# Performance work log

Measured on AMD Instinct MI355X. Metric: run time of the kernel, lower is better.

The kernel has to match this reference:

```python
import jax, jax.numpy as jnp
import numpy as np

C = 512
GROUPS = 32
EPS = 1e-6


def setup_inputs() -> dict:
    key = jax.random.key(0)
    ks = jax.random.split(key, 10)
    B, H, W = 4, 64, 64
    s = 1.0 / np.sqrt(C)
    return {
        "x": jax.random.normal(ks[0], (B, C, H, W), dtype=jnp.float32),
        "gn_weight": jnp.ones((C,), jnp.float32),
        "gn_bias": jnp.zeros((C,), jnp.float32),
        "Wq": jax.random.normal(ks[1], (C, C), jnp.float32) * s,
        "bq": jnp.zeros((C,), jnp.float32),
        "Wk": jax.random.normal(ks[2], (C, C), jnp.float32) * s,
        "bk": jnp.zeros((C,), jnp.float32),
        "Wv": jax.random.normal(ks[3], (C, C), jnp.float32) * s,
        "bv": jnp.zeros((C,), jnp.float32),
        "Wo": jax.random.normal(ks[4], (C, C), jnp.float32) * s,
        "bo": jnp.zeros((C,), jnp.float32),
    }


def _group_norm(x, weight, bias):
    B, Ch, H, W = x.shape
    xg = x.reshape(B, GROUPS, Ch // GROUPS, H, W)
    mean = jnp.mean(xg, axis=(2, 3, 4), keepdims=True)
    var = jnp.var(xg, axis=(2, 3, 4), keepdims=True)
    xg = (xg - mean) * jax.lax.rsqrt(var + EPS)
    h = xg.reshape(B, Ch, H, W)
    return h * weight[None, :, None, None] + bias[None, :, None, None]


def reference(x, gn_weight, gn_bias, Wq, bq, Wk, bk, Wv, bv, Wo, bo):
    B, Ch, H, W = x.shape
    h = _group_norm(x, gn_weight, gn_bias)
    # [B, N, C] with N = H*W spatial tokens
    h = h.reshape(B, Ch, H * W).transpose(0, 2, 1)
    q = h @ Wq.T + bq
    k = h @ Wk.T + bk
    v = h @ Wv.T + bv
    scale = 1.0 / jnp.sqrt(jnp.asarray(Ch, x.dtype))
    scores = jnp.einsum("bnc,bmc->bnm", q, k) * scale  # [B, N, N]
    attn = jax.nn.softmax(scores, axis=-1)
    out = jnp.einsum("bnm,bmc->bnc", attn, v)
    out = out @ Wo.T + bo  # Dropout(0.0) is identity
    out = out.transpose(0, 2, 1).reshape(B, Ch, H, W)
    return x + out
```

## Files before the change

### kernel.cpp

```cpp
#include <hip/hip_runtime.h>
#include <hip/hip_bf16.h>

typedef __attribute__((ext_vector_type(8))) short bf16x8;
typedef __attribute__((ext_vector_type(4))) short bf16x4;
typedef __attribute__((ext_vector_type(4))) float f32x4;

__device__ __forceinline__ short f2bf(float f){
  __hip_bfloat16 h = __float2bfloat16(f);
  return __builtin_bit_cast(short, h);
}
__device__ __forceinline__ float bf2f(short s){
  unsigned u = ((unsigned)(unsigned short)s) << 16;
  return __builtin_bit_cast(float, u);
}

__device__ __forceinline__ void gload_lds16(const short* g, char* l){
  __builtin_amdgcn_global_load_lds(
      (const __attribute__((address_space(1))) void*)g,
      (__attribute__((address_space(3))) void*)l, 16, 0, 0);
}

__global__ __launch_bounds__(256) void gn_stats(const float* __restrict__ x,
                                                float* __restrict__ stats){
  int b = blockIdx.x >> 5, g = blockIdx.x & 31;
  const float4* p = (const float4*)(x + ((long long)b*512 + g*16)*4096);
  float s = 0.f, s2 = 0.f;
  for (int i = threadIdx.x; i < 16384; i += 256){
    float4 v = p[i];
    s  += v.x + v.y + v.z + v.w;
    s2 += v.x*v.x + v.y*v.y + v.z*v.z + v.w*v.w;
  }
  #pragma unroll
  for (int o = 32; o; o >>= 1){ s += __shfl_xor(s, o); s2 += __shfl_xor(s2, o); }
  __shared__ float rs[4], rs2[4];
  int wid = threadIdx.x >> 6;
  if ((threadIdx.x & 63) == 0){ rs[wid] = s; rs2[wid] = s2; }
  __syncthreads();
  if (threadIdx.x == 0){
    float S  = rs[0]+rs[1]+rs[2]+rs[3];
    float S2 = rs2[0]+rs2[1]+rs2[2]+rs2[3];
    float mean = S * (1.f/65536.f);
    float var  = S2 * (1.f/65536.f) - mean*mean;
    stats[blockIdx.x*2]   = mean;
    stats[blockIdx.x*2+1] = rsqrtf(var + 1e-6f);
  }
}

__global__ __launch_bounds__(256) void gn_apply(const float* __restrict__ x,
                                                const float* __restrict__ stats,
                                                const float* __restrict__ gw,
                                                const float* __restrict__ gb,
                                                short* __restrict__ h){
  __shared__ float tile[128][65];
  int b  = blockIdx.y;
  int n0 = blockIdx.x * 64;
  int t  = threadIdx.x;
  const float* xb = x + (long long)b*512*4096;
  for (int cc = 0; cc < 4; cc++){
    int c0 = cc*128;
    #pragma unroll
    for (int r = 0; r < 128; r += 4){
      int c = r + (t >> 6);
      tile[c][t & 63] = xb[(long long)(c0+c)*4096 + n0 + (t & 63)];
    }
    __syncthreads();
    int n = t >> 2, cp = (t & 3)*32;
    short tmp[32];
    #pragma unroll
    for (int j = 0; j < 32; j++){
      int c = c0 + cp + j;
      float mean = stats[(b*32 + (c >> 4))*2];
      float rstd = stats[(b*32 + (c >> 4))*2 + 1];
      float v = (tile[cp+j][n] - mean)*rstd*gw[c] + gb[c];
      tmp[j] = f2bf(v);
    }
    long long ho = ((long long)b*4096 + n0 + n)*512 + c0 + cp;
    #pragma unroll
    for (int j2 = 0; j2 < 4; j2++){
      bf16x8 v8;
      #pragma unroll
      for (int e = 0; e < 8; e++) v8[e] = tmp[j2*8 + e];
      *(bf16x8*)&h[ho + j2*8] = v8;
    }
    __syncthreads();
  }
}

__global__ __launch_bounds__(256) void f2bf_all(
    const float* __restrict__ w0, const float* __restrict__ w1,
    const float* __restrict__ w2, const float* __restrict__ w3,
    short* __restrict__ o0, short* __restrict__ o1,
    short* __restrict__ o2, short* __restrict__ o3){
  int idx = blockIdx.x*256 + threadIdx.x;
  int m = idx >> 15, r = idx & 32767;
  const float* src = (m==0) ? w0 : (m==1) ? w1 : (m==2) ? w2 : w3;
  short* dst       = (m==0) ? o0 : (m==1) ? o1 : (m==2) ? o2 : o3;
  const float4* p = (const float4*)src + (long long)r*2;
  float4 a = p[0], c = p[1];
  bf16x8 v;
  v[0]=f2bf(a.x); v[1]=f2bf(a.y); v[2]=f2bf(a.z); v[3]=f2bf(a.w);
  v[4]=f2bf(c.x); v[5]=f2bf(c.y); v[6]=f2bf(c.z); v[7]=f2bf(c.w);
  *(bf16x8*)&dst[(long long)r*8] = v;
}

__global__ __launch_bounds__(256) void softmax_rows(short* __restrict__ S){
  long long row = blockIdx.x;
  short* p = S + row*4096;
  int t = threadIdx.x;
  bf16x8 v0 = *(bf16x8*)&p[t*16];
  bf16x8 v1 = *(bf16x8*)&p[t*16 + 8];
  float f[16];
  #pragma unroll
  for (int e = 0; e < 8; e++){ f[e] = bf2f(v0[e]); f[8+e] = bf2f(v1[e]); }
  float m = f[0];
  #pragma unroll
  for (int e = 1; e < 16; e++) m = fmaxf(m, f[e]);
  #pragma unroll
  for (int o = 32; o; o >>= 1) m = fmaxf(m, __shfl_xor(m, o));
  __shared__ float red[4];
  int wid = t >> 6;
  if ((t & 63) == 0) red[wid] = m;
  __syncthreads();
  m = fmaxf(fmaxf(red[0], red[1]), fmaxf(red[2], red[3]));
  float s = 0.f;
  #pragma unroll
  for (int e = 0; e < 16; e++){ f[e] = exp2f((f[e]-m)*1.4426950408889634f); s += f[e]; }
  #pragma unroll
  for (int o = 32; o; o >>= 1) s += __shfl_xor(s, o);
  __syncthreads();
  if ((t & 63) == 0) red[wid] = s;
  __syncthreads();
  s = red[0]+red[1]+red[2]+red[3];
  float inv = 1.f/s;
  #pragma unroll
  for (int e = 0; e < 8; e++){ v0[e] = f2bf(f[e]*inv); v1[e] = f2bf(f[8+e]*inv); }
  *(bf16x8*)&p[t*16]     = v0;
  *(bf16x8*)&p[t*16 + 8] = v1;
}

template<int MODE, int BN>
__global__ __launch_bounds__(512, 2) void gemm256(
    const short* __restrict__ A, const short* __restrict__ Bw,
    const float* __restrict__ bias,
    void* __restrict__ outp, const float* __restrict__ resid,
    int M, int Nn, int Kd,
    long long sA, long long sB, long long sO, float scale)
{
  constexpr int BROUNDS = BN/64;
  constexpr int LOADS   = 4 + BROUNDS;
  constexpr int WM = (BN==256) ? 128 : 64;
  constexpr int WN = 64;
  constexpr int WAVES_N = BN/WN;
  constexpr int MF = WM/16, NF = WN/16;
  constexpr int ASZ = 32768, BSZ = BN*128;
  extern __shared__ char smem[];

  const int bz = blockIdx.z;
  const short* Ab = A + bz*sA;
  const short* Bb = Bw + bz*sB;
  const int m0 = blockIdx.x*256, n0 = blockIdx.y*BN;
  const int t = threadIdx.x;
  const int lane = t & 63, wid = t >> 6;
  const int g = lane >> 4, lr = lane & 15;
  const int wr = wid / WAVES_N, wc = wid % WAVES_N;

  const int rsub = t >> 3;
  const int chunkEl = (((t & 7) ^ (rsub & 7))) * 8;
  const short* gA[4]; const short* gB[BROUNDS];
  #pragma unroll
  for (int j = 0; j < 4; j++)
    gA[j] = Ab + (long long)(m0 + j*64 + rsub)*Kd + chunkEl;
  #pragma unroll
  for (int j = 0; j < BROUNDS; j++)
    gB[j] = Bb + (long long)(n0 + j*64 + rsub)*Kd + chunkEl;
  const int tb = t*16;

  const int rowAbyte = (wr*WM + lr)*128;
  const int rowBbyte = (wc*WN + lr)*128;
  const int ch0 = ((g)     ^ (lr & 7)) << 4;
  const int ch1 = ((4 + g) ^ (lr & 7)) << 4;

  f32x4 acc[MF][NF];
  #pragma unroll
  for (int i = 0; i < MF; i++)
    #pragma unroll
    for (int j = 0; j < NF; j++)
      acc[i][j] = f32x4{0.f,0.f,0.f,0.f};

  const int NT = Kd >> 6;

  auto STAGE = [&](int tile, int buf){
    char* base = smem + buf*(ASZ+BSZ);
    const int kt = tile*64;
    #pragma unroll
    for (int j = 0; j < 4; j++)
      gload_lds16(gA[j] + kt, base + j*8192 + tb);
    #pragma unroll
    for (int j = 0; j < BROUNDS; j++)
      gload_lds16(gB[j] + kt, base + ASZ + j*8192 + tb);
  };

  STAGE(0, 0);
  STAGE(1, 1);
  if constexpr (LOADS == 8) asm volatile("s_waitcnt vmcnt(8)" ::: "memory");
  else                      asm volatile("s_waitcnt vmcnt(6)" ::: "memory");
  __builtin_amdgcn_s_barrier();

  for (int it = 0; it < NT; ++it){
    char* base = smem + (it & 1)*(ASZ+BSZ);
    bf16x8 av[MF][2], bv[NF][2];
    #pragma unroll
    for (int ni = 0; ni < NF; ni++){
      bv[ni][0] = *(const bf16x8*)(base + ASZ + rowBbyte + ni*2048 + ch0);
      bv[ni][1] = *(const bf16x8*)(base + ASZ + rowBbyte + ni*2048 + ch1);
    }
    #pragma unroll
    for (int mi = 0; mi < MF; mi++){
      av[mi][0] = *(const bf16x8*)(base + rowAbyte + mi*2048 + ch0);
      av[mi][1] = *(const bf16x8*)(base + rowAbyte + mi*2048 + ch1);
    }
    asm volatile("s_waitcnt lgkmcnt(0)" ::: "memory");
    __builtin_amdgcn_sched_barrier(0);
    __builtin_amdgcn_s_barrier();

    if (it + 2 < NT) STAGE(it + 2, it & 1);

    #pragma unroll
    for (int mi = 0; mi < MF; mi++)
      #pragma unroll
      for (int ni = 0; ni < NF; ni++)
        #pragma unroll
        for (int ks = 0; ks < 2; ks++){
          if constexpr (MODE == 0)
            acc[mi][ni] = __builtin_amdgcn_mfma_f32_16x16x32_bf16(bv[ni][ks], av[mi][ks], acc[mi][ni], 0, 0, 0);
          else
            acc[mi][ni] = __builtin_amdgcn_mfma_f32_16x16x32_bf16(av[mi][ks], bv[ni][ks], acc[mi][ni], 0, 0, 0);
        }

    if (it + 2 < NT){
      if constexpr (LOADS == 8) asm volatile("s_waitcnt vmcnt(8)" ::: "memory");
      else                      asm volatile("s_waitcnt vmcnt(6)" ::: "memory");
    } else {
      asm volatile("s_waitcnt vmcnt(0)" ::: "memory");
    }
    __builtin_amdgcn_s_barrier();
  }

  if constexpr (MODE == 0){
    short* outb = (short*)outp + bz*sO;
    const bool hb = (bias != nullptr);
    #pragma unroll
    for (int mi = 0; mi < MF; mi++){
      int row = m0 + wr*WM + mi*16 + lr;
      #pragma unroll
      for (int ni = 0; ni < NF; ni++){
        int col = n0 + wc*WN + ni*16 + g*4;
        float b0=0.f,b1=0.f,b2=0.f,b3=0.f;
        if (hb){ float4 bb = *(const float4*)&bias[col]; b0=bb.x; b1=bb.y; b2=bb.z; b3=bb.w; }
        bf16x4 pk;
        pk[0] = f2bf((acc[mi][ni][0] + b0)*scale);
        pk[1] = f2bf((acc[mi][ni][1] + b1)*scale);
        pk[2] = f2bf((acc[mi][ni][2] + b2)*scale);
        pk[3] = f2bf((acc[mi][ni][3] + b3)*scale);
        *(bf16x4*)&outb[(long long)row*Nn + col] = pk;
      }
    }
  } else if constexpr (MODE == 1){
    short* outb = (short*)outp + bz*sO;
    #pragma unroll
    for (int ni = 0; ni < NF; ni++){
      int col = n0 + wc*WN + ni*16 + lr;
      float bv2 = bias ? bias[col] : 0.f;
      #pragma unroll
      for (int mi = 0; mi < MF; mi++){
        int row = m0 + wr*WM + mi*16 + g*4;
        bf16x4 pk;
        #pragma unroll
        for (int i = 0; i < 4; i++) pk[i] = f2bf((acc[mi][ni][i] + bv2)*scale);
        *(bf16x4*)&outb[(long long)col*M + row] = pk;
      }
    }
  } else {
    float* outb = (float*)outp + bz*sO;
    const float* rx = resid + bz*sO;
    #pragma unroll
    for (int ni = 0; ni < NF; ni++){
      int col = n0 + wc*WN + ni*16 + lr;
      float bv2 = bias[col];
      #pragma unroll
      for (int mi = 0; mi < MF; mi++){
        int row = m0 + wr*WM + mi*16 + g*4;
        long long off = (long long)col*M + row;
        float4 xr = *(const float4*)&rx[off];
        float4 o;
        o.x = acc[mi][ni][0] + bv2 + xr.x;
        o.y = acc[mi][ni][1] + bv2 + xr.y;
        o.z = acc[mi][ni][2] + bv2 + xr.z;
        o.w = acc[mi][ni][3] + bv2 + xr.w;
        *(float4*)&outb[off] = o;
      }
    }
  }
}

extern "C" void kernel_launch(void* const* d_in, const int* in_sizes, int n_in,
                              void* d_out, int out_size, void* d_ws, size_t ws_size,
                              hipStream_t stream)
{
  const float* x   = (const float*)d_in[0];
  const float* gnw = (const float*)d_in[1];
  const float* gnb = (const float*)d_in[2];
  const float* Wq  = (const float*)d_in[3];
  const float* bq  = (const float*)d_in[4];
  const float* Wk  = (const float*)d_in[5];
  const float* bk  = (const float*)d_in[6];
  const float* Wv  = (const float*)d_in[7];
  const float* bvp = (const float*)d_in[8];
  const float* Wo  = (const float*)d_in[9];
  const float* bo  = (const float*)d_in[10];
  float* out = (float*)d_out;

  char* ws = (char*)d_ws;
  const size_t MB = 1ull << 20;
  short* h    = (short*)(ws);
  short* q    = (short*)(ws + 16*MB);
  short* kmat = (short*)(ws + 32*MB);
  short* vt   = (short*)(ws + 48*MB);
  short* ao   = (short*)(ws + 64*MB);
  short* wqb  = (short*)(ws + 80*MB);
  short* wkb  = wqb + 262144;
  short* wvb  = wkb + 262144;
  short* wob  = wvb + 262144;
  float* stats= (float*)(ws + 82*MB);
  short* S    = (short*)(ws + 84*MB);

  const int LDS256 = 131072, LDS128 = 98304;
  hipFuncSetAttribute(reinterpret_cast<const void*>(&gemm256<0,256>),
                      hipFuncAttributeMaxDynamicSharedMemorySize, LDS256);
  hipFuncSetAttribute(reinterpret_cast<const void*>(&gemm256<0,128>),
                      hipFuncAttributeMaxDynamicSharedMemorySize, LDS128);
  hipFuncSetAttribute(reinterpret_cast<const void*>(&gemm256<1,128>),
                      hipFuncAttributeMaxDynamicSharedMemorySize, LDS128);
  hipFuncSetAttribute(reinterpret_cast<const void*>(&gemm256<2,128>),
                      hipFuncAttributeMaxDynamicSharedMemorySize, LDS128);

  dim3 blk(256);
  dim3 blk512(512);
  gn_stats<<<dim3(128), blk, 0, stream>>>(x, stats);
  gn_apply<<<dim3(64,4), blk, 0, stream>>>(x, stats, gnw, gnb, h);
  f2bf_all<<<dim3(512), blk, 0, stream>>>(Wq, Wk, Wv, Wo, wqb, wkb, wvb, wob);

  const long long sTok = 4096ll*512;
  const float qscale = 0.044194173824159216f;

  gemm256<0,128><<<dim3(16,4,4), blk512, LDS128, stream>>>(h, wqb, bq,  q,    nullptr, 4096, 512, 512, sTok, 0, sTok, qscale);
  gemm256<0,128><<<dim3(16,4,4), blk512, LDS128, stream>>>(h, wkb, bk,  kmat, nullptr, 4096, 512, 512, sTok, 0, sTok, 1.f);
  gemm256<1,128><<<dim3(16,4,4), blk512, LDS128, stream>>>(h, wvb, bvp, vt,   nullptr, 4096, 512, 512, sTok, 0, sTok, 1.f);

  if (ws_size >= 212*MB){
    gemm256<0,256><<<dim3(16,16,4), blk512, LDS256, stream>>>(q, kmat, nullptr, S, nullptr, 4096, 4096, 512, sTok, sTok, 4096ll*4096, 1.f);
    softmax_rows<<<dim3(16384), blk, 0, stream>>>(S);
    gemm256<0,128><<<dim3(16,4,4), blk512, LDS128, stream>>>(S, vt, nullptr, ao, nullptr, 4096, 512, 4096, 4096ll*4096, sTok, sTok, 1.f);
  } else {
    for (int b = 0; b < 4; b++){
      gemm256<0,256><<<dim3(16,16,1), blk512, LDS256, stream>>>(q + b*sTok, kmat + b*sTok, nullptr, S, nullptr, 4096, 4096, 512, 0, 0, 0, 1.f);
      softmax_rows<<<dim3(4096), blk, 0, stream>>>(S);
      gemm256<0,128><<<dim3(16,4,1), blk512, LDS128, stream>>>(S, vt + b*sTok, nullptr, ao + b*sTok, nullptr, 4096, 512, 4096, 0, 0, 0, 1.f);
    }
  }

  gemm256<2,128><<<dim3(16,4,4), blk512, LDS128, stream>>>(ao, wob, bo, out, x, 4096, 512, 512, sTok, 0, sTok, 1.f);
}
```

Measured before the change: 352.7 us.

## Add 8-phase pipelined GEMM kernel for attention score and PV matmuls

Adds a new gemm8p kernel that splits each K-tile into four MFMA quadrants, interleaving LDS reads and async global-to-LDS staging with compute phases separated by barriers and s_setprio. It uses double-buffered LDS with fine-grained vmcnt waits so loads overlap with MFMA work. The QK^T and softmax×V GEMMs now use it in place of gemm256. The hand-scheduled barriers and waitcnt logic add complexity and could stall if the phases are mismatched.

```diff
diff --git a/kernel.cpp b/kernel.cpp
--- a/kernel.cpp
+++ b/kernel.cpp
@@ -136,6 +136,190 @@
   for (int e = 0; e < 8; e++){ v0[e] = f2bf(f[e]*inv); v1[e] = f2bf(f[8+e]*inv); }
   *(bf16x8*)&p[t*16]     = v0;
   *(bf16x8*)&p[t*16 + 8] = v1;
+}
+
+#define READ_A8(QM, BASE) do{                                          \
+  _Pragma("unroll")                                                    \
+  for (int _i = 0; _i < MF2; _i++){                                    \
+    _Pragma("unroll")                                                  \
+    for (int _ks = 0; _ks < 2; _ks++)                                  \
+      av[_i][_ks] = *(const bf16x8*)((BASE) + roA[(QM)*MF2+_i] +       \
+                     (((_ks*4+g) ^ swA[(QM)*MF2+_i])<<4));             \
+  } }while(0)
+
+#define READ_B4(QN, BASE) do{                                          \
+  _Pragma("unroll")                                                    \
+  for (int _j = 0; _j < 2; _j++){                                      \
+    _Pragma("unroll")                                                  \
+    for (int _ks = 0; _ks < 2; _ks++)                                  \
+      bv[(QN)*2+_j][_ks] = *(const bf16x8*)((BASE) + roB[(QN)*2+_j] +  \
+                     (((_ks*4+g) ^ swB[(QN)*2+_j])<<4));               \
+  } }while(0)
+
+#define MFMA_Q(QM, QN) do{                                             \
+  _Pragma("unroll")                                                    \
+  for (int _i = 0; _i < MF2; _i++)                                     \
+    _Pragma("unroll")                                                  \
+    for (int _j = 0; _j < 2; _j++)                                     \
+      _Pragma("unroll")                                                \
+      for (int _ks = 0; _ks < 2; _ks++)                                \
+        acc[(QM)*MF2+_i][(QN)*2+_j] =                                  \
+          __builtin_amdgcn_mfma_f32_16x16x32_bf16(bv[(QN)*2+_j][_ks],  \
+            av[_i][_ks], acc[(QM)*MF2+_i][(QN)*2+_j], 0,0,0);          \
+  }while(0)
+
+#define STAGE_A(BUF, H, KT) do{                                        \
+  char* _d = smem + (BUF)*BUFSZ + (H)*16384 + t*16;                    \
+  const short* _s = pA0 + (H)*128*KdLL + (KT)*64;                      \
+  gload_lds16(_s, _d);                                                 \
+  gload_lds16(_s + 64*KdLL, _d + 8192);                                \
+}while(0)
+
+#define STAGE_B(BUF, H, KT) do{                                        \
+  char* _d = smem + (BUF)*BUFSZ + ABUF + (H)*BHALF + t*16;             \
+  const short* _s = pB0 + (H)*RB*KdLL + (KT)*64;                       \
+  gload_lds16(_s, _d);                                                 \
+  if constexpr (LB == 2) gload_lds16(_s + 64*KdLL, _d + 8192);         \
+}while(0)
+
+#define WAITV_STEADY() do{                                             \
+  if constexpr (LB == 2) asm volatile("s_waitcnt vmcnt(4)" ::: "memory"); \
+  else                   asm volatile("s_waitcnt vmcnt(2)" ::: "memory"); \
+}while(0)
+
+#define PH_BEGIN()                                                     \
+  __builtin_amdgcn_sched_barrier(0);                                   \
+  __builtin_amdgcn_s_barrier();                                        \
+  __builtin_amdgcn_sched_barrier(0);                                   \
+  asm volatile("s_waitcnt lgkmcnt(0)" ::: "memory");                   \
+  __builtin_amdgcn_sched_barrier(0);                                   \
+  __builtin_amdgcn_s_setprio(1)
+
+#define PH_END()                                                       \
+  __builtin_amdgcn_s_setprio(0);                                       \
+  __builtin_amdgcn_sched_barrier(0);                                   \
+  __builtin_amdgcn_s_barrier()
+
+template<int BN>
+__global__ __launch_bounds__(512, 2) void gemm8p(
+    const short* __restrict__ A, const short* __restrict__ Bw,
+    short* __restrict__ outp,
+    int Nn, int Kd,
+    long long sA, long long sB, long long sO, float scale)
+{
+  constexpr int WN = 64;
+  constexpr int WARPS_N = BN/WN;
+  constexpr int WARPS_M = 8/WARPS_N;
+  constexpr int WM = 256/WARPS_M;
+  constexpr int MF = WM/16;
+  constexpr int MF2 = MF/2;
+  constexpr int ABUF = 32768;
+  constexpr int BBUF = BN*128;
+  constexpr int BHALF = BBUF/2;
+  constexpr int RB = BHALF/128;
+  constexpr int LB = BHALF/8192;
+  constexpr int BUFSZ = ABUF + BBUF;
+  extern __shared__ char smem[];
+
+  const int bz = blockIdx.z;
+  const short* Ab = A + bz*sA;
+  const short* Bb = Bw + bz*sB;
+  const int m0 = blockIdx.x*256, n0 = blockIdx.y*BN;
+  const int t = threadIdx.x;
+  const int lane = t & 63, wid = t >> 6;
+  const int g = lane >> 4, lr = lane & 15;
+  const int wr = wid / WARPS_N, wc = wid % WARPS_N;
+  const long long KdLL = Kd;
+
+  const int r0 = t >> 3;
+  const int c0s = ((t & 7) ^ (r0 & 7)) * 8;
+  const short* pA0 = Ab + (long long)(m0 + r0)*KdLL + c0s;
+  const short* pB0 = Bb + (long long)(n0 + r0)*KdLL + c0s;
+
+  int roA[MF], swA[MF], roB[4], swB[4];
+  #pragma unroll
+  for (int mf = 0; mf < MF; mf++){
+    int ra = wr*WM + mf*16 + lr;
+    roA[mf] = (ra>>7)*16384 + (ra&127)*128;
+    swA[mf] = ra & 7;
+  }
+  #pragma unroll
+  for (int nf = 0; nf < 4; nf++){
+    int cb = wc*WN + nf*16 + lr;
+    roB[nf] = ABUF + (cb/RB)*BHALF + (cb%RB)*128;
+    swB[nf] = cb & 7;
+  }
+
+  f32x4 acc[MF][4];
+  #pragma unroll
+  for (int i = 0; i < MF; i++)
+    #pragma unroll
+    for (int j = 0; j < 4; j++)
+      acc[i][j] = f32x4{0.f,0.f,0.f,0.f};
+  bf16x8 av[MF2][2], bv[4][2];
+
+  char* b0 = smem;
+  char* b1 = smem + BUFSZ;
+  const int NT = Kd >> 6;
+  const int NT2 = NT >> 1;
+
+  STAGE_A(0,0,0); STAGE_A(0,1,0);
+  STAGE_B(0,0,0); STAGE_B(0,1,0);
+  STAGE_B(1,0,1); STAGE_B(1,1,1);
+  WAITV_STEADY();
+  __builtin_amdgcn_sched_barrier(0);
+  __builtin_amdgcn_s_barrier();
+
+  for (int it2 = 0; it2 < NT2; ++it2){
+    const int kt0 = it2*2, kt1 = kt0 + 1;
+    const bool more = (it2 + 1 < NT2);
+    READ_A8(0, b0); READ_B4(0, b0);
+    STAGE_A(1, 0, kt1);
+    PH_BEGIN(); MFMA_Q(0,0); PH_END();
+    READ_B4(1, b0);
+    STAGE_A(1, 1, kt1);
+    PH_BEGIN(); MFMA_Q(0,1); PH_END();
+    READ_A8(1, b0);
+    if (more) STAGE_B(0, 0, kt0+2);
+    PH_BEGIN(); MFMA_Q(1,0); PH_END();
+    if (more) STAGE_B(0, 1, kt0+2);
+    PH_BEGIN(); MFMA_Q(1,1);
+    __builtin_amdgcn_s_setprio(0);
+    if (more) WAITV_STEADY();
+    else      asm volatile("s_waitcnt vmcnt(0)" ::: "memory");
+    __builtin_amdgcn_sched_barrier(0);
+    __builtin_amdgcn_s_barrier();
+    READ_A8(0, b1); READ_B4(0, b1);
+    if (more) STAGE_A(0, 0, kt0+2);
+    PH_BEGIN(); MFMA_Q(0,0); PH_END();
+    READ_B4(1, b1);
+    if (more) STAGE_A(0, 1, kt0+2);
+    PH_BEGIN(); MFMA_Q(0,1); PH_END();
+    READ_A8(1, b1);
+    if (more) STAGE_B(1, 0, kt1+2);
+    PH_BEGIN(); MFMA_Q(1,0); PH_END();
+    if (more) STAGE_B(1, 1, kt1+2);
+    PH_BEGIN(); MFMA_Q(1,1);
+    __builtin_amdgcn_s_setprio(0);
+    if (more) WAITV_STEADY();
+    else      asm volatile("s_waitcnt vmcnt(0)" ::: "memory");
+    __builtin_amdgcn_sched_barrier(0);
+    __builtin_amdgcn_s_barrier();
+  }
+
+  short* outb = outp + bz*sO;
+  #pragma unroll
+  for (int mi = 0; mi < MF; mi++){
+    int row = m0 + wr*WM + mi*16 + lr;
+    #pragma unroll
+    for (int ni = 0; ni < 4; ni++){
+      int col = n0 + wc*WN + ni*16 + g*4;
+      bf16x4 pk;
+      #pragma unroll
+      for (int i = 0; i < 4; i++) pk[i] = f2bf(acc[mi][ni][i]*scale);
+      *(bf16x4*)&outb[(long long)row*Nn + col] = pk;
+    }
+  }
 }
 
 template<int MODE, int BN>
@@ -334,9 +518,11 @@
   float* stats= (float*)(ws + 82*MB);
   short* S    = (short*)(ws + 84*MB);
 
-  const int LDS256 = 131072, LDS128 = 98304;
-  hipFuncSetAttribute(reinterpret_cast<const void*>(&gemm256<0,256>),
-                      hipFuncAttributeMaxDynamicSharedMemorySize, LDS256);
+  const int LDS8P256 = 131072, LDS8P128 = 98304, LDS128 = 98304;
+  hipFuncSetAttribute(reinterpret_cast<const void*>(&gemm8p<256>),
+                      hipFuncAttributeMaxDynamicSharedMemorySize, LDS8P256);
+  hipFuncSetAttribute(reinterpret_cast<const void*>(&gemm8p<128>),
+                      hipFuncAttributeMaxDynamicSharedMemorySize, LDS8P128);
   hipFuncSetAttribute(reinterpret_cast<const void*>(&gemm256<0,128>),
                       hipFuncAttributeMaxDynamicSharedMemorySize, LDS128);
   hipFuncSetAttribute(reinterpret_cast<const void*>(&gemm256<1,128>),
@@ -358,14 +544,14 @@
   gemm256<1,128><<<dim3(16,4,4), blk512, LDS128, stream>>>(h, wvb, bvp, vt,   nullptr, 4096, 512, 512, sTok, 0, sTok, 1.f);
 
   if (ws_size >= 212*MB){
-    gemm256<0,256><<<dim3(16,16,4), blk512, LDS256, stream>>>(q, kmat, nullptr, S, nullptr, 4096, 4096, 512, sTok, sTok, 4096ll*4096, 1.f);
+    gemm8p<256><<<dim3(16,16,4), blk512, LDS8P256, stream>>>(q, kmat, S, 4096, 512, sTok, sTok, 4096ll*4096, 1.f);
     softmax_rows<<<dim3(16384), blk, 0, stream>>>(S);
-    gemm256<0,128><<<dim3(16,4,4), blk512, LDS128, stream>>>(S, vt, nullptr, ao, nullptr, 4096, 512, 4096, 4096ll*4096, sTok, sTok, 1.f);
+    gemm8p<128><<<dim3(16,4,4), blk512, LDS8P128, stream>>>(S, vt, ao, 512, 4096, 4096ll*4096, sTok, sTok, 1.f);
   } else {
     for (int b = 0; b < 4; b++){
-      gemm256<0,256><<<dim3(16,16,1), blk512, LDS256, stream>>>(q + b*sTok, kmat + b*sTok, nullptr, S, nullptr, 4096, 4096, 512, 0, 0, 0, 1.f);
+      gemm8p<256><<<dim3(16,16,1), blk512, LDS8P256, stream>>>(q + b*sTok, kmat + b*sTok, S, 4096, 512, 0, 0, 0, 1.f);
       softmax_rows<<<dim3(4096), blk, 0, stream>>>(S);
-      gemm256<0,128><<<dim3(16,4,1), blk512, LDS128, stream>>>(S, vt + b*sTok, nullptr, ao + b*sTok, nullptr, 4096, 512, 4096, 0, 0, 0, 1.f);
+      gemm8p<128><<<dim3(16,4,1), blk512, LDS8P128, stream>>>(S, vt + b*sTok, ao + b*sTok, 512, 4096, 0, 0, 0, 1.f);
     }
   }
 
```

New measurement: 340.0 us. 1.04x faster.

## Interleave LDS fragment reads with MFMA quadrants and swizzle score-GEMM blocks

Applied to the files above, without the earlier changes.

The GEMM main loop now splits the warp tile into four MFMA quadrants. LDS fragment reads are issued in pieces with partial lgkmcnt waits, so matrix math starts before all operands arrive. MFMA bursts run at raised wave priority, and the next tile's global-to-LDS prefetch is issued mid-iteration. The QK^T score GEMM also gets a 1-D grid remapped so that each XCD (selected by the low block-id bits) works on a compact 4x4 tile region, for better L2 reuse of Q and K. The tradeoff is more scheduling barriers, more register pressure and tighter hand-tuned ordering.

```diff
diff --git a/kernel.cpp b/kernel.cpp
--- a/kernel.cpp
+++ b/kernel.cpp
@@ -19,6 +19,10 @@
       (const __attribute__((address_space(1))) void*)g,
       (__attribute__((address_space(3))) void*)l, 16, 0, 0);
 }
+
+#define SB0() __builtin_amdgcn_sched_barrier(0)
+#define LGKM0() do{ asm volatile("s_waitcnt lgkmcnt(0)" ::: "memory"); SB0(); }while(0)
+#define LGKM4() do{ asm volatile("s_waitcnt lgkmcnt(4)" ::: "memory"); SB0(); }while(0)
 
 __global__ __launch_bounds__(256) void gn_stats(const float* __restrict__ x,
                                                 float* __restrict__ stats){
@@ -138,111 +142,151 @@
   *(bf16x8*)&p[t*16 + 8] = v1;
 }
 
-template<int MODE, int BN>
-__global__ __launch_bounds__(512, 2) void gemm256(
+template<int MODE, int BN, bool SWZ>
+__global__ __launch_bounds__(512, 2) void gemmP(
     const short* __restrict__ A, const short* __restrict__ Bw,
     const float* __restrict__ bias,
     void* __restrict__ outp, const float* __restrict__ resid,
     int M, int Nn, int Kd,
     long long sA, long long sB, long long sO, float scale)
 {
-  constexpr int BROUNDS = BN/64;
-  constexpr int LOADS   = 4 + BROUNDS;
-  constexpr int WM = (BN==256) ? 128 : 64;
   constexpr int WN = 64;
-  constexpr int WAVES_N = BN/WN;
-  constexpr int MF = WM/16, NF = WN/16;
-  constexpr int ASZ = 32768, BSZ = BN*128;
+  constexpr int WARPS_N = BN/WN;
+  constexpr int WARPS_M = 8/WARPS_N;
+  constexpr int WM = 256/WARPS_M;
+  constexpr int MF = WM/16;
+  constexpr int MF2 = MF/2;
+  constexpr int ABUF = 32768;
+  constexpr int BBUF = BN*128;
+  constexpr int BUFSZ = ABUF + BBUF;
+  constexpr int BLOADS = BN/64;
+  constexpr int LOADS = 4 + BLOADS;
   extern __shared__ char smem[];
 
-  const int bz = blockIdx.z;
+  int bx, by, bz;
+  if constexpr (SWZ){
+    int id = blockIdx.x;
+    int c = id & 7, s = id >> 3;
+    int region = c + ((s >> 4) << 3);
+    int o = s & 15;
+    bz = region >> 4;
+    bx = (region & 3)*4 + (o & 3);
+    by = ((region >> 2) & 3)*4 + (o >> 2);
+  } else { bx = blockIdx.x; by = blockIdx.y; bz = blockIdx.z; }
+
   const short* Ab = A + bz*sA;
   const short* Bb = Bw + bz*sB;
-  const int m0 = blockIdx.x*256, n0 = blockIdx.y*BN;
+  const int m0 = bx*256, n0 = by*BN;
   const int t = threadIdx.x;
   const int lane = t & 63, wid = t >> 6;
   const int g = lane >> 4, lr = lane & 15;
-  const int wr = wid / WAVES_N, wc = wid % WAVES_N;
-
-  const int rsub = t >> 3;
-  const int chunkEl = (((t & 7) ^ (rsub & 7))) * 8;
-  const short* gA[4]; const short* gB[BROUNDS];
-  #pragma unroll
-  for (int j = 0; j < 4; j++)
-    gA[j] = Ab + (long long)(m0 + j*64 + rsub)*Kd + chunkEl;
-  #pragma unroll
-  for (int j = 0; j < BROUNDS; j++)
-    gB[j] = Bb + (long long)(n0 + j*64 + rsub)*Kd + chunkEl;
-  const int tb = t*16;
-
-  const int rowAbyte = (wr*WM + lr)*128;
-  const int rowBbyte = (wc*WN + lr)*128;
-  const int ch0 = ((g)     ^ (lr & 7)) << 4;
-  const int ch1 = ((4 + g) ^ (lr & 7)) << 4;
-
-  f32x4 acc[MF][NF];
+  const int wr = wid / WARPS_N, wc = wid % WARPS_N;
+  const long long KdLL = Kd;
+
+  const int r0 = t >> 3;
+  const int c0s = ((t & 7) ^ (r0 & 7)) * 8;
+  const short* pA0 = Ab + (long long)(m0 + r0)*KdLL + c0s;
+  const short* pB0 = Bb + (long long)(n0 + r0)*KdLL + c0s;
+
+  int roA[MF], swA[MF], roB[4], swB[4];
+  #pragma unroll
+  for (int mf = 0; mf < MF; mf++){
+    int ra = wr*WM + mf*16 + lr;
+    roA[mf] = ra*128; swA[mf] = ra & 7;
+  }
+  #pragma unroll
+  for (int nf = 0; nf < 4; nf++){
+    int cb = wc*WN + nf*16 + lr;
+    roB[nf] = ABUF + cb*128; swB[nf] = cb & 7;
+  }
+
+  f32x4 acc[MF][4];
   #pragma unroll
   for (int i = 0; i < MF; i++)
     #pragma unroll
-    for (int j = 0; j < NF; j++)
+    for (int j = 0; j < 4; j++)
       acc[i][j] = f32x4{0.f,0.f,0.f,0.f};
+  bf16x8 av[MF2][2], bv[4][2];
+
+  auto STAGE = [&](int kt, int buf){
+    char* d = smem + buf*BUFSZ;
+    const short* sa = pA0 + (long long)kt*64;
+    #pragma unroll
+    for (int j = 0; j < 4; j++)
+      gload_lds16(sa + (long long)j*64*KdLL, d + j*8192 + t*16);
+    const short* sb = pB0 + (long long)kt*64;
+    #pragma unroll
+    for (int j = 0; j < BLOADS; j++)
+      gload_lds16(sb + (long long)j*64*KdLL, d + ABUF + j*8192 + t*16);
+  };
+
+  #define RD_AV(HI)                                                          \
+    _Pragma("unroll")                                                        \
+    for (int i = 0; i < MF2; i++){                                           \
+      _Pragma("unroll")                                                      \
+      for (int ks = 0; ks < 2; ks++)                                         \
+        av[i][ks] = *(const bf16x8*)(base + roA[(HI)*MF2+i] +                \
+                      ((((ks<<2)+g) ^ swA[(HI)*MF2+i])<<4));                 \
+    }
+  #define RD_BV(J0)                                                          \
+    _Pragma("unroll")                                                        \
+    for (int j = 0; j < 2; j++){                                             \
+      _Pragma("unroll")                                                      \
+      for (int ks = 0; ks < 2; ks++)                                         \
+        bv[(J0)+j][ks] = *(const bf16x8*)(base + roB[(J0)+j] +               \
+                      ((((ks<<2)+g) ^ swB[(J0)+j])<<4));                     \
+    }
+  #define QUAD(QM, QN)                                                       \
+    __builtin_amdgcn_s_setprio(1);                                           \
+    _Pragma("unroll")                                                        \
+    for (int i = 0; i < MF2; i++)                                            \
+      _Pragma("unroll")                                                      \
+      for (int j = 0; j < 2; j++)                                            \
+        _Pragma("unroll")                                                    \
+        for (int ks = 0; ks < 2; ks++){                                      \
+          if constexpr (MODE == 0)                                           \
+            acc[(QM)*MF2+i][(QN)*2+j] = __builtin_amdgcn_mfma_f32_16x16x32_bf16( \
+              bv[(QN)*2+j][ks], av[i][ks], acc[(QM)*MF2+i][(QN)*2+j], 0,0,0);\
+          else                                                               \
+            acc[(QM)*MF2+i][(QN)*2+j] = __builtin_amdgcn_mfma_f32_16x16x32_bf16( \
+              av[i][ks], bv[(QN)*2+j][ks], acc[(QM)*MF2+i][(QN)*2+j], 0,0,0);\
+        }                                                                    \
+    __builtin_amdgcn_s_setprio(0);
 
   const int NT = Kd >> 6;
-
-  auto STAGE = [&](int tile, int buf){
-    char* base = smem + buf*(ASZ+BSZ);
-    const int kt = tile*64;
-    #pragma unroll
-    for (int j = 0; j < 4; j++)
-      gload_lds16(gA[j] + kt, base + j*8192 + tb);
-    #pragma unroll
-    for (int j = 0; j < BROUNDS; j++)
-      gload_lds16(gB[j] + kt, base + ASZ + j*8192 + tb);
-  };
 
   STAGE(0, 0);
   STAGE(1, 1);
   if constexpr (LOADS == 8) asm volatile("s_waitcnt vmcnt(8)" ::: "memory");
   else                      asm volatile("s_waitcnt vmcnt(6)" ::: "memory");
+  SB0();
   __builtin_amdgcn_s_barrier();
 
   for (int it = 0; it < NT; ++it){
-    char* base = smem + (it & 1)*(ASZ+BSZ);
-    bf16x8 av[MF][2], bv[NF][2];
-    #pragma unroll
-    for (int ni = 0; ni < NF; ni++){
-      bv[ni][0] = *(const bf16x8*)(base + ASZ + rowBbyte + ni*2048 + ch0);
-      bv[ni][1] = *(const bf16x8*)(base + ASZ + rowBbyte + ni*2048 + ch1);
-    }
-    #pragma unroll
-    for (int mi = 0; mi < MF; mi++){
-      av[mi][0] = *(const bf16x8*)(base + rowAbyte + mi*2048 + ch0);
-      av[mi][1] = *(const bf16x8*)(base + rowAbyte + mi*2048 + ch1);
-    }
-    asm volatile("s_waitcnt lgkmcnt(0)" ::: "memory");
-    __builtin_amdgcn_sched_barrier(0);
+    char* base = smem + (it & 1)*BUFSZ;
+    const bool more = (it + 2 < NT);
+    RD_AV(0); RD_BV(0); SB0();
+    RD_BV(2); SB0();
+    LGKM4();
+    QUAD(0,0);
+    LGKM0();
+    QUAD(0,1);
+    SB0();
+    RD_AV(1); SB0();
+    LGKM0();
+    QUAD(1,0);
+    SB0();
     __builtin_amdgcn_s_barrier();
-
-    if (it + 2 < NT) STAGE(it + 2, it & 1);
-
-    #pragma unroll
-    for (int mi = 0; mi < MF; mi++)
-      #pragma unroll
-      for (int ni = 0; ni < NF; ni++)
-        #pragma unroll
-        for (int ks = 0; ks < 2; ks++){
-          if constexpr (MODE == 0)
-            acc[mi][ni] = __builtin_amdgcn_mfma_f32_16x16x32_bf16(bv[ni][ks], av[mi][ks], acc[mi][ni], 0, 0, 0);
-          else
-            acc[mi][ni] = __builtin_amdgcn_mfma_f32_16x16x32_bf16(av[mi][ks], bv[ni][ks], acc[mi][ni], 0, 0, 0);
-        }
-
-    if (it + 2 < NT){
+    if (more) STAGE(it + 2, it & 1);
+    QUAD(1,1);
+    SB0();
+    if (more){
       if constexpr (LOADS == 8) asm volatile("s_waitcnt vmcnt(8)" ::: "memory");
       else                      asm volatile("s_waitcnt vmcnt(6)" ::: "memory");
     } else {
       asm volatile("s_waitcnt vmcnt(0)" ::: "memory");
     }
+    SB0();
     __builtin_amdgcn_s_barrier();
   }
 
@@ -253,7 +297,7 @@
     for (int mi = 0; mi < MF; mi++){
       int row = m0 + wr*WM + mi*16 + lr;
       #pragma unroll
-      for (int ni = 0; ni < NF; ni++){
+      for (int ni = 0; ni < 4; ni++){
         int col = n0 + wc*WN + ni*16 + g*4;
         float b0=0.f,b1=0.f,b2=0.f,b3=0.f;
         if (hb){ float4 bb = *(const float4*)&bias[col]; b0=bb.x; b1=bb.y; b2=bb.z; b3=bb.w; }
@@ -268,7 +312,7 @@
   } else if constexpr (MODE == 1){
     short* outb = (short*)outp + bz*sO;
     #pragma unroll
-    for (int ni = 0; ni < NF; ni++){
+    for (int ni = 0; ni < 4; ni++){
       int col = n0 + wc*WN + ni*16 + lr;
       float bv2 = bias ? bias[col] : 0.f;
       #pragma unroll
@@ -284,7 +328,7 @@
     float* outb = (float*)outp + bz*sO;
     const float* rx = resid + bz*sO;
     #pragma unroll
-    for (int ni = 0; ni < NF; ni++){
+    for (int ni = 0; ni < 4; ni++){
       int col = n0 + wc*WN + ni*16 + lr;
       float bv2 = bias[col];
       #pragma unroll
@@ -301,6 +345,9 @@
       }
     }
   }
+  #undef RD_AV
+  #undef RD_BV
+  #undef QUAD
 }
 
 extern "C" void kernel_launch(void* const* d_in, const int* in_sizes, int n_in,
@@ -335,13 +382,13 @@
   short* S    = (short*)(ws + 84*MB);
 
   const int LDS256 = 131072, LDS128 = 98304;
-  hipFuncSetAttribute(reinterpret_cast<const void*>(&gemm256<0,256>),
+  hipFuncSetAttribute(reinterpret_cast<const void*>(&gemmP<0,256,true>),
                       hipFuncAttributeMaxDynamicSharedMemorySize, LDS256);
-  hipFuncSetAttribute(reinterpret_cast<const void*>(&gemm256<0,128>),
+  hipFuncSetAttribute(reinterpret_cast<const void*>(&gemmP<0,128,false>),
                       hipFuncAttributeMaxDynamicSharedMemorySize, LDS128);
-  hipFuncSetAttribute(reinterpret_cast<const void*>(&gemm256<1,128>),
+  hipFuncSetAttribute(reinterpret_cast<const void*>(&gemmP<1,128,false>),
                       hipFuncAttributeMaxDynamicSharedMemorySize, LDS128);
-  hipFuncSetAttribute(reinterpret_cast<const void*>(&gemm256<2,128>),
+  hipFuncSetAttribute(reinterpret_cast<const void*>(&gemmP<2,128,false>),
                       hipFuncAttributeMaxDynamicSharedMemorySize, LDS128);
 
   dim3 blk(256);
@@ -351,23 +398,24 @@
   f2bf_all<<<dim3(512), blk, 0, stream>>>(Wq, Wk, Wv, Wo, wqb, wkb, wvb, wob);
 
   const long long sTok = 4096ll*512;
+  const long long sS   = 4096ll*4096;
   const float qscale = 0.044194173824159216f;
 
-  gemm256<0,128><<<dim3(16,4,4), blk512, LDS128, stream>>>(h, wqb, bq,  q,    nullptr, 4096, 512, 512, sTok, 0, sTok, qscale);
-  gemm256<0,128><<<dim3(16,4,4), blk512, LDS128, stream>>>(h, wkb, bk,  kmat, nullptr, 4096, 512, 512, sTok, 0, sTok, 1.f);
-  gemm256<1,128><<<dim3(16,4,4), blk512, LDS128, stream>>>(h, wvb, bvp, vt,   nullptr, 4096, 512, 512, sTok, 0, sTok, 1.f);
+  gemmP<0,128,false><<<dim3(16,4,4), blk512, LDS128, stream>>>(h, wqb, bq,  q,    nullptr, 4096, 512, 512, sTok, 0, sTok, qscale);
+  gemmP<0,128,false><<<dim3(16,4,4), blk512, LDS128, stream>>>(h, wkb, bk,  kmat, nullptr, 4096, 512, 512, sTok, 0, sTok, 1.f);
+  gemmP<1,128,false><<<dim3(16,4,4), blk512, LDS128, stream>>>(h, wvb, bvp, vt,   nullptr, 4096, 512, 512, sTok, 0, sTok, 1.f);
 
   if (ws_size >= 212*MB){
-    gemm256<0,256><<<dim3(16,16,4), blk512, LDS256, stream>>>(q, kmat, nullptr, S, nullptr, 4096, 4096, 512, sTok, sTok, 4096ll*4096, 1.f);
+    gemmP<0,256,true><<<dim3(1024), blk512, LDS256, stream>>>(q, kmat, nullptr, S, nullptr, 4096, 4096, 512, sTok, sTok, sS, 1.f);
     softmax_rows<<<dim3(16384), blk, 0, stream>>>(S);
-    gemm256<0,128><<<dim3(16,4,4), blk512, LDS128, stream>>>(S, vt, nullptr, ao, nullptr, 4096, 512, 4096, 4096ll*4096, sTok, sTok, 1.f);
+    gemmP<0,128,false><<<dim3(16,4,4), blk512, LDS128, stream>>>(S, vt, nullptr, ao, nullptr, 4096, 512, 4096, sS, sTok, sTok, 1.f);
   } else {
     for (int b = 0; b < 4; b++){
-      gemm256<0,256><<<dim3(16,16,1), blk512, LDS256, stream>>>(q + b*sTok, kmat + b*sTok, nullptr, S, nullptr, 4096, 4096, 512, 0, 0, 0, 1.f);
+      gemmP<0,256,true><<<dim3(256), blk512, LDS256, stream>>>(q + b*sTok, kmat + b*sTok, nullptr, S, nullptr, 4096, 4096, 512, 0, 0, 0, 1.f);
       softmax_rows<<<dim3(4096), blk, 0, stream>>>(S);
-      gemm256<0,128><<<dim3(16,4,1), blk512, LDS128, stream>>>(S, vt + b*sTok, nullptr, ao + b*sTok, nullptr, 4096, 512, 4096, 0, 0, 0, 1.f);
-    }
-  }
-
-  gemm256<2,128><<<dim3(16,4,4), blk512, LDS128, stream>>>(ao, wob, bo, out, x, 4096, 512, 512, sTok, 0, sTok, 1.f);
-}
+      gemmP<0,128,false><<<dim3(16,4,1), blk512, LDS128, stream>>>(S, vt + b*sTok, nullptr, ao + b*sTok, nullptr, 4096, 512, 4096, 0, 0, 0, 1.f);
+    }
+  }
+
+  gemmP<2,128,false><<<dim3(16,4,4), blk512, LDS128, stream>>>(ao, wob, bo, out, x, 4096, 512, 512, sTok, 0, sTok, 1.f);
+}
```

Result: faster. 344.3 us (-2.4%).
